# Kernel optimization log

Measured on AMD Instinct MI355X. Metric: run time of the kernel, lower is better.

Reference implementation:

```python
import jax, jax.numpy as jnp
import numpy as np

B, D_IN, H, D_OUT, E = 16384, 512, 1024, 512, 4


def setup_inputs() -> dict:
    key = jax.random.key(0)
    ks = jax.random.split(key, 8)
    x = jax.random.normal(ks[0], (B, D_IN), dtype=jnp.float32)
    command = jax.random.randint(ks[1], (B,), 0, E, dtype=jnp.int64)
    # Per-branch Encoder params: Linear(D_IN->H), Linear(H->H), Linear(H->D_OUT)
    s = 0.02
    W1 = jax.random.normal(ks[2], (E, D_IN, H), dtype=jnp.float32) * s
    b1 = jnp.zeros((E, H), dtype=jnp.float32)
    W2 = jax.random.normal(ks[3], (E, H, H), dtype=jnp.float32) * s
    b2 = jnp.zeros((E, H), dtype=jnp.float32)
    W3 = jax.random.normal(ks[4], (E, H, D_OUT), dtype=jnp.float32) * s
    b3 = jnp.zeros((E, D_OUT), dtype=jnp.float32)
    return {"x": x, "command": command, "W1": W1, "b1": b1,
            "W2": W2, "b2": b2, "W3": W3, "b3": b3}


def reference(x, command, W1, b1, W2, b2, W3, b3):
    # Evaluate all branches as batched GEMMs, then select per-sample branch.
    # Mathematically identical to per-sample dispatch in the torch module.
    h = jax.nn.relu(jnp.einsum('bi,eih->beh', x, W1) + b1)        # [B,E,H]
    h = jax.nn.relu(jnp.einsum('beh,ehk->bek', h, W2) + b2)       # [B,E,H]
    y = jnp.tanh(jnp.einsum('bek,eko->beo', h, W3) + b3)          # [B,E,D_OUT]
    # select branch output per sample according to command
    idx = command.astype(jnp.int32)[:, None, None]                # [B,1,1]
    out = jnp.take_along_axis(y, idx, axis=1)[:, 0, :]            # [B,D_OUT]
    return out
```

## Files before the change

### kernel.cpp

```cpp
#include <hip/hip_runtime.h>


#define B_N   16384
#define DIN   512
#define HID   1024
#define DOUT  512
#define MAXTILES 136

typedef __attribute__((ext_vector_type(8))) short bf16x8;
typedef __attribute__((ext_vector_type(4))) float f32x4;
typedef __attribute__((address_space(3))) unsigned int lds_u32;
typedef const __attribute__((address_space(1))) unsigned int glb_u32;

__device__ __forceinline__ void gll16(const void* g, void* l) {
    __builtin_amdgcn_global_load_lds((glb_u32*)g, (lds_u32*)l, 16, 0, 0);
}

__device__ __forceinline__ unsigned short f2bf(float f) {
    unsigned int u = __float_as_uint(f);
    u += 0x7FFFu + ((u >> 16) & 1u);
    return (unsigned short)(u >> 16);
}

__device__ __forceinline__ float fast_tanh(float x) {
    x = fminf(fmaxf(x, -9.0f), 9.0f);
    float t = __builtin_amdgcn_exp2f(x * 2.8853900817779268f);
    return (t - 1.0f) * __builtin_amdgcn_rcpf(t + 1.0f);
}

__global__ void plan_all_k(const int* __restrict__ cmd, int* __restrict__ ctrl,
                           int* __restrict__ tileExpert, int* __restrict__ tileBase) {
    __shared__ int h[4];
    int tid = threadIdx.x;
    if (tid < 4) h[tid] = 0;
    __syncthreads();
    int c0 = 0, c1 = 0, c2 = 0, c3 = 0;
    for (int i = tid; i < B_N; i += 256) {
        int e = cmd[i] & 3;
        c0 += (e == 0); c1 += (e == 1); c2 += (e == 2); c3 += (e == 3);
    }
    atomicAdd(&h[0], c0); atomicAdd(&h[1], c1);
    atomicAdd(&h[2], c2); atomicAdd(&h[3], c3);
    __syncthreads();
    if (tid == 0) {
        int P = 0, nt = 0;
        for (int e = 0; e < 4; ++e) {
            ctrl[e] = h[e];
            ctrl[4 + e] = 0;
            ctrl[8 + e] = P;
            int tiles = (h[e] + 127) >> 7;
            for (int t = 0; t < tiles; ++t) {
                tileExpert[nt] = e;
                tileBase[nt] = P + t * 128;
                ++nt;
            }
            P += tiles * 128;
        }
        ctrl[12] = P;
        ctrl[13] = nt;
    }
}

__global__ void scatter_k(const int* __restrict__ cmd, int* __restrict__ ctrl,
                          int* __restrict__ perm) {
    int i = blockIdx.x * 256 + threadIdx.x;
    int e = cmd[i] & 3;
    int lane = threadIdx.x & 63;
#pragma unroll
    for (int ee = 0; ee < 4; ++ee) {
        unsigned long long mask = __ballot(e == ee);
        if (e == ee) {
            int leader = __ffsll((unsigned long long)mask) - 1;
            int rank = __popcll(mask & ((1ull << lane) - 1ull));
            int wbase = 0;
            if (lane == leader)
                wbase = atomicAdd(&ctrl[4 + ee], __popcll(mask));
            wbase = __builtin_amdgcn_readfirstlane(wbase);
            perm[ctrl[8 + ee] + wbase + rank] = i;
        }
    }
}

__global__ __launch_bounds__(256) void prep_data_k(
    const float* __restrict__ W1, const float* __restrict__ W2,
    const float* __restrict__ W3, unsigned short* __restrict__ Wt1,
    unsigned short* __restrict__ Wt2, unsigned short* __restrict__ Wt3,
    const float* __restrict__ x, unsigned short* __restrict__ xp,
    int* __restrict__ perm, const int* __restrict__ ctrl)
{
    int b = blockIdx.x;
    if (b < 8192) {
        int e = b >> 11, r = b & 2047;
        const float* W; unsigned short* Wt; int KD, ND, kt, nt;
        if (r < 512)       { W = W1; Wt = Wt1; KD = 512;  ND = 1024; kt = r & 15;           nt = r >> 4; }
        else if (r < 1536) { W = W2; Wt = Wt2; KD = 1024; ND = 1024; kt = (r - 512) & 31;   nt = (r - 512) >> 5; }
        else               { W = W3; Wt = Wt3; KD = 1024; ND = 512;  kt = (r - 1536) & 31;  nt = (r - 1536) >> 5; }
        __shared__ float t[32][33];
        size_t base = (size_t)e * KD * ND;
        int k0 = kt * 32, n0 = nt * 32;
        int tx = threadIdx.x & 31, ty = threadIdx.x >> 5;
#pragma unroll
        for (int s = 0; s < 4; ++s)
            t[ty + s * 8][tx] = W[base + (size_t)(k0 + ty + s * 8) * ND + n0 + tx];
        __syncthreads();
#pragma unroll
        for (int s = 0; s < 4; ++s)
            Wt[base + (size_t)(n0 + ty + s * 8) * KD + k0 + tx] = f2bf(t[tx][ty + s * 8]);
    } else {
        int g = b - 8192;
        int p = g * 4 + (int)(threadIdx.x >> 6);
        if (p >= ctrl[12]) return;
        int lane = threadIdx.x & 63;
        int e = (p >= ctrl[9]) + (p >= ctrl[10]) + (p >= ctrl[11]);
        int segBase = ctrl[8 + e];
        int src;
        if (p < segBase + ctrl[e]) {
            src = perm[p];
        } else {
            src = perm[segBase];
            if (lane == 0) perm[p] = src;
        }
        const float* xr = x + (size_t)src * DIN + lane * 8;
        float4 a = *(const float4*)xr;
        float4 c = *(const float4*)(xr + 4);
        uint4 o;
        o.x = (unsigned)f2bf(a.x) | ((unsigned)f2bf(a.y) << 16);
        o.y = (unsigned)f2bf(a.z) | ((unsigned)f2bf(a.w) << 16);
        o.z = (unsigned)f2bf(c.x) | ((unsigned)f2bf(c.y) << 16);
        o.w = (unsigned)f2bf(c.z) | ((unsigned)f2bf(c.w) << 16);
        *(uint4*)(xp + (size_t)p * DIN + lane * 8) = o;
    }
}

template<int K, int N, int ACT, bool SCATTER_OUT>
__global__ __launch_bounds__(256) void gemm_k(
    const unsigned short* __restrict__ A, const unsigned short* __restrict__ Bt,
    const float* __restrict__ bias, void* __restrict__ Outp,
    const int* __restrict__ ctrl, const int* __restrict__ tileExpert,
    const int* __restrict__ tileBase, const int* __restrict__ perm)
{
    if ((int)blockIdx.x >= ctrl[13]) return;
    const int e = tileExpert[blockIdx.x];
    const int rowBase = tileBase[blockIdx.x];
    const int n0 = blockIdx.y * 128;

    __shared__ unsigned short Als[2][128 * 32];
    __shared__ unsigned short Bls[2][128 * 32];

    const int tid = threadIdx.x;
    const int lane = tid & 63;
    const int w = tid >> 6;
    const int wm = w >> 1, wn = w & 1;
    const int lr = lane & 15, lh = lane >> 4;

    f32x4 acc[4][4] = {};

    const int sr = tid >> 2;
    const int sc = (tid & 3) * 8;
    const int l1 = sr * 32 + sc;
    const int l2 = (sr + 64) * 32 + sc;
    const unsigned short* Ab1 = A + (size_t)(rowBase + sr) * K + sc;
    const unsigned short* Ab2 = A + (size_t)(rowBase + sr + 64) * K + sc;
    const unsigned short* Bb1 = Bt + ((size_t)e * N + n0 + sr) * K + sc;
    const unsigned short* Bb2 = Bt + ((size_t)e * N + n0 + sr + 64) * K + sc;

    constexpr int NK = K / 32;
#define STAGE(buf, kb) do {                                   \
        const int _k0 = (kb) * 32;                            \
        gll16(Ab1 + _k0, &Als[buf][l1]);                      \
        gll16(Ab2 + _k0, &Als[buf][l2]);                      \
        gll16(Bb1 + _k0, &Bls[buf][l1]);                      \
        gll16(Bb2 + _k0, &Bls[buf][l2]);                      \
    } while (0)

    STAGE(0, 0);
#pragma unroll 2
    for (int kb = 0; kb < NK; ++kb) {
        const int cur = kb & 1;
        asm volatile("s_waitcnt vmcnt(0)" ::: "memory");
        __builtin_amdgcn_s_barrier();
        asm volatile("" ::: "memory");
        if (kb + 1 < NK) STAGE(cur ^ 1, kb + 1);
        bf16x8 afr[4], bfr[4];
#pragma unroll
        for (int mi = 0; mi < 4; ++mi)
            afr[mi] = *(const bf16x8*)&Als[cur][(wm * 64 + mi * 16 + lr) * 32 + lh * 8];
#pragma unroll
        for (int ni = 0; ni < 4; ++ni)
            bfr[ni] = *(const bf16x8*)&Bls[cur][(wn * 64 + ni * 16 + lr) * 32 + lh * 8];
#pragma unroll
        for (int mi = 0; mi < 4; ++mi)
#pragma unroll
            for (int ni = 0; ni < 4; ++ni)
                acc[mi][ni] = __builtin_amdgcn_mfma_f32_16x16x32_bf16(
                    afr[mi], bfr[ni], acc[mi][ni], 0, 0, 0);
    }
#undef STAGE

    float bv[4];
    int colv[4];
#pragma unroll
    for (int ni = 0; ni < 4; ++ni) {
        colv[ni] = n0 + wn * 64 + ni * 16 + lr;
        bv[ni] = bias[e * N + colv[ni]];
    }
#pragma unroll
    for (int mi = 0; mi < 4; ++mi) {
#pragma unroll
        for (int r = 0; r < 4; ++r) {
            int rowL = wm * 64 + mi * 16 + lh * 4 + r;
            int gRow = rowBase + rowL;
            int orow = SCATTER_OUT ? perm[gRow] : gRow;
#pragma unroll
            for (int ni = 0; ni < 4; ++ni) {
                float v = acc[mi][ni][r] + bv[ni];
                if (ACT == 0) v = fmaxf(v, 0.0f);
                else          v = fast_tanh(v);
                if (SCATTER_OUT)
                    ((float*)Outp)[(size_t)orow * N + colv[ni]] = v;
                else
                    ((unsigned short*)Outp)[(size_t)orow * N + colv[ni]] = f2bf(v);
            }
        }
    }
}

extern "C" void kernel_launch(void* const* d_in, const int* in_sizes, int n_in,
                              void* d_out, int out_size, void* d_ws, size_t ws_size,
                              hipStream_t stream) {
    const float* x  = (const float*)d_in[0];
    const int*   cmd= (const int*)d_in[1];
    const float* W1 = (const float*)d_in[2];
    const float* b1 = (const float*)d_in[3];
    const float* W2 = (const float*)d_in[4];
    const float* b2 = (const float*)d_in[5];
    const float* W3 = (const float*)d_in[6];
    const float* b3 = (const float*)d_in[7];
    float* out = (float*)d_out;

    char* w = (char*)d_ws;
    int* ctrl       = (int*)w;
    int* tileExpert = ctrl + 64;
    int* tileBase   = ctrl + 224;
    int* perm       = ctrl + 512;
    unsigned short* Wt1 = (unsigned short*)(w + 131072);
    unsigned short* Wt2 = (unsigned short*)(w + 131072 + 4194304);
    unsigned short* Wt3 = (unsigned short*)(w + 131072 + 12582912);
    unsigned short* h1  = (unsigned short*)(w + 131072 + 16777216);
    unsigned short* h2  = h1 + (size_t)16896 * HID;
    unsigned short* xp  = h2;

    plan_all_k<<<1, 256, 0, stream>>>(cmd, ctrl, tileExpert, tileBase);
    scatter_k<<<B_N / 256, 256, 0, stream>>>(cmd, ctrl, perm);
    prep_data_k<<<8192 + 4224, 256, 0, stream>>>(W1, W2, W3, Wt1, Wt2, Wt3,
                                                 x, xp, perm, ctrl);

    gemm_k<DIN, HID, 0, false><<<dim3(MAXTILES, 8), 256, 0, stream>>>(
        xp, Wt1, b1, h1, ctrl, tileExpert, tileBase, perm);
    gemm_k<HID, HID, 0, false><<<dim3(MAXTILES, 8), 256, 0, stream>>>(
        h1, Wt2, b2, h2, ctrl, tileExpert, tileBase, perm);
    gemm_k<HID, DOUT, 1, true><<<dim3(MAXTILES, 4), 256, 0, stream>>>(
        h2, Wt3, b3, out, ctrl, tileExpert, tileBase, perm);
}
```

Before: 186.3 us.

## Deepen GEMM LDS pipeline to 4 stages with XOR swizzle and MFMA priority

```diff
diff --git a/kernel.cpp b/kernel.cpp
--- a/kernel.cpp
+++ b/kernel.cpp
@@ -144,8 +144,8 @@
     const int rowBase = tileBase[blockIdx.x];
     const int n0 = blockIdx.y * 128;
 
-    __shared__ unsigned short Als[2][128 * 32];
-    __shared__ unsigned short Bls[2][128 * 32];
+    __shared__ unsigned short Als[4 * 4096];
+    __shared__ unsigned short Bls[4 * 4096];
 
     const int tid = threadIdx.x;
     const int lane = tid & 63;
@@ -155,47 +155,66 @@
 
     f32x4 acc[4][4] = {};
 
-    const int sr = tid >> 2;
-    const int sc = (tid & 3) * 8;
-    const int l1 = sr * 32 + sc;
-    const int l2 = (sr + 64) * 32 + sc;
-    const unsigned short* Ab1 = A + (size_t)(rowBase + sr) * K + sc;
-    const unsigned short* Ab2 = A + (size_t)(rowBase + sr + 64) * K + sc;
-    const unsigned short* Bb1 = Bt + ((size_t)e * N + n0 + sr) * K + sc;
-    const unsigned short* Bb2 = Bt + ((size_t)e * N + n0 + sr + 64) * K + sc;
-
-    constexpr int NK = K / 32;
-#define STAGE(buf, kb) do {                                   \
-        const int _k0 = (kb) * 32;                            \
-        gll16(Ab1 + _k0, &Als[buf][l1]);                      \
-        gll16(Ab2 + _k0, &Als[buf][l2]);                      \
-        gll16(Bb1 + _k0, &Bls[buf][l1]);                      \
-        gll16(Bb2 + _k0, &Bls[buf][l2]);                      \
-    } while (0)
-
-    STAGE(0, 0);
-#pragma unroll 2
-    for (int kb = 0; kb < NK; ++kb) {
-        const int cur = kb & 1;
-        asm volatile("s_waitcnt vmcnt(0)" ::: "memory");
-        __builtin_amdgcn_s_barrier();
-        asm volatile("" ::: "memory");
-        if (kb + 1 < NK) STAGE(cur ^ 1, kb + 1);
+    const int tr = tid >> 2;
+    const int tc = tid & 3;
+    const int cs = (tc ^ ((tr >> 1) & 3)) * 8;
+    const unsigned short* As0 = A + (size_t)(rowBase + tr) * K + cs;
+    const unsigned short* As1 = As0 + (size_t)64 * K;
+    const unsigned short* Bs0 = Bt + ((size_t)e * N + n0 + tr) * K + cs;
+    const unsigned short* Bs1 = Bs0 + (size_t)64 * K;
+    const int ld0 = tid * 8;
+    const int ld1 = 2048 + tid * 8;
+    const int ksl = (lh ^ ((lr >> 1) & 3)) * 8;
+
+    auto STAGE = [&](int t) {
+        const int k0 = t * 32;
+        const int sb = (t & 3) * 4096;
+        gll16(As0 + k0, &Als[sb + ld0]);
+        gll16(As1 + k0, &Als[sb + ld1]);
+        gll16(Bs0 + k0, &Bls[sb + ld0]);
+        gll16(Bs1 + k0, &Bls[sb + ld1]);
+    };
+    auto COMPUTE = [&](int t) {
+        const int sb = (t & 3) * 4096;
         bf16x8 afr[4], bfr[4];
 #pragma unroll
         for (int mi = 0; mi < 4; ++mi)
-            afr[mi] = *(const bf16x8*)&Als[cur][(wm * 64 + mi * 16 + lr) * 32 + lh * 8];
+            afr[mi] = *(const bf16x8*)&Als[sb + (wm * 64 + mi * 16 + lr) * 32 + ksl];
 #pragma unroll
         for (int ni = 0; ni < 4; ++ni)
-            bfr[ni] = *(const bf16x8*)&Bls[cur][(wn * 64 + ni * 16 + lr) * 32 + lh * 8];
+            bfr[ni] = *(const bf16x8*)&Bls[sb + (wn * 64 + ni * 16 + lr) * 32 + ksl];
+        __builtin_amdgcn_s_setprio(1);
 #pragma unroll
         for (int mi = 0; mi < 4; ++mi)
 #pragma unroll
             for (int ni = 0; ni < 4; ++ni)
                 acc[mi][ni] = __builtin_amdgcn_mfma_f32_16x16x32_bf16(
                     afr[mi], bfr[ni], acc[mi][ni], 0, 0, 0);
-    }
-#undef STAGE
+        __builtin_amdgcn_s_setprio(0);
+    };
+
+    constexpr int NK = K / 32;
+    STAGE(0); STAGE(1); STAGE(2);
+    for (int t = 0; t < NK - 3; ++t) {
+        __builtin_amdgcn_s_barrier();
+        STAGE(t + 3);
+        asm volatile("s_waitcnt vmcnt(12)" ::: "memory");
+        __builtin_amdgcn_s_barrier();
+        __builtin_amdgcn_sched_barrier(0);
+        COMPUTE(t);
+    }
+    asm volatile("s_waitcnt vmcnt(8)" ::: "memory");
+    __builtin_amdgcn_s_barrier();
+    __builtin_amdgcn_sched_barrier(0);
+    COMPUTE(NK - 3);
+    asm volatile("s_waitcnt vmcnt(4)" ::: "memory");
+    __builtin_amdgcn_s_barrier();
+    __builtin_amdgcn_sched_barrier(0);
+    COMPUTE(NK - 2);
+    asm volatile("s_waitcnt vmcnt(0)" ::: "memory");
+    __builtin_amdgcn_s_barrier();
+    __builtin_amdgcn_sched_barrier(0);
+    COMPUTE(NK - 1);
 
     float bv[4];
     int colv[4];
```

Result: slower. 198.3 us (+6.5%).
